# Kernel tuning notes

Hardware: AMD Instinct MI355X
Metric: run time of the kernel (lower is better)

## Reference

```python
import jax, jax.numpy as jnp
import numpy as np

CAP_FACTOR = 0.125  # capacity_factor from init_kwargs


def setup_inputs() -> dict:
    key = jax.random.key(0)
    k1, k2, k3, k4 = jax.random.split(key, 4)
    B, S, D, F = 4, 4096, 1024, 4096
    x = jax.random.normal(k1, (B, S, D), jnp.float32)
    w_router = jax.random.normal(k2, (D,), jnp.float32) * (D ** -0.5)
    W1 = jax.random.normal(k3, (D, F), jnp.float32) * (D ** -0.5)
    W2 = jax.random.normal(k4, (F, D), jnp.float32) * (F ** -0.5)
    return {"x": x, "w_router": w_router, "W1": W1, "W2": W2}


def reference(x, w_router, W1, W2):
    B, S, D = x.shape
    capacity = int(S * CAP_FACTOR)  # training-mode capacity (static)

    # router: Linear(dim,1,bias=False) + sigmoid -> [B, S]
    rw = jax.nn.sigmoid(jnp.einsum('bsd,d->bs', x, w_router))

    # topk over seq dim, then sort selected indices
    _, top_idx = jax.lax.top_k(rw, capacity)          # [B, cap]
    idx_sorted = jnp.sort(top_idx, axis=1)            # router_top_indices
    order = jnp.argsort(top_idx, axis=1)              # router_top_order (in [0, cap))

    # faithful to the original code: weights gathered from router_weights at
    # `order` positions (which index the first `capacity` sequence slots)
    w_top = jnp.take_along_axis(rw, order, axis=1)    # [B, cap]

    # gather selected tokens and run the submodule (gelu MLP)
    mod_x = jnp.take_along_axis(x, idx_sorted[:, :, None], axis=1)  # [B, cap, D]
    h = jax.nn.gelu(jnp.einsum('bcd,df->bcf', mod_x, W1))
    mod_out = jnp.einsum('bcf,fd->bcd', h, W2) * w_top[:, :, None]

    # scatter back to full sequence (indices are unique per batch)
    bidx = jnp.arange(B)[:, None]
    out = jnp.zeros_like(x).at[bidx, idx_sorted].set(mod_out)

    # BCE aux loss: targets are 1 at selected positions (log clamped at -100,
    # matching F.binary_cross_entropy)
    tgt = jnp.zeros_like(rw).at[bidx, idx_sorted].set(1.0)
    logw = jnp.maximum(jnp.log(rw), -100.0)
    log1mw = jnp.maximum(jnp.log1p(-rw), -100.0)
    mod_loss = -jnp.mean(tgt * logw + (1.0 - tgt) * log1mw)

    return out, mod_loss
```

## Files before the change

### kernel.cpp

```cpp
#include <hip/hip_runtime.h>
#include <stdint.h>

#define BB 4
#define SS 4096
#define DD 1024
#define FF 4096
#define CAP 512
#define MTOT (BB*CAP)
#define NOUT (BB*SS*DD)

typedef unsigned short ushort_t;
typedef float  float4v  __attribute__((ext_vector_type(4)));
typedef short  short8v  __attribute__((ext_vector_type(8)));
typedef unsigned short ushort4v __attribute__((ext_vector_type(4)));

#define OFF_RW   0u
#define OFF_IDX  (64u*1024u)
#define OFF_WTOP (72u*1024u)
#define OFF_LOSS (80u*1024u)
#define OFF_POS  (128u*1024u)
#define OFF_RANK (256u*1024u)
#define OFF_A    (1u<<20)
#define OFF_W1T  (5u<<20)
#define OFF_W2T  (13u<<20)
#define OFF_H    (21u<<20)
#define OFF_O    (37u<<20)

#define GLD16(gsrc, ldst) __builtin_amdgcn_global_load_lds( \
    (const __attribute__((address_space(1))) void*)(gsrc),  \
    (__attribute__((address_space(3))) void*)(ldst), 16, 0, 0)

__device__ inline ushort_t f2bf(float f) {
  uint32_t u = __builtin_bit_cast(uint32_t, f);
  u = u + 0x7fffu + ((u >> 16) & 1u);
  return (ushort_t)(u >> 16);
}
__device__ inline float bf2f(ushort_t h) {
  uint32_t u = (uint32_t)h << 16;
  return __builtin_bit_cast(float, u);
}

__global__ void router_kernel(const float* __restrict__ x, const float* __restrict__ w,
                              float* __restrict__ rw) {
  int wave = threadIdx.x >> 6;
  int lane = threadIdx.x & 63;
  int row  = blockIdx.x * 4 + wave;
  const float4* xr = (const float4*)(x + (size_t)row * DD);
  const float4* wr = (const float4*)w;
  float s = 0.f;
#pragma unroll
  for (int i = 0; i < 4; i++) {
    float4 a = xr[lane + i * 64];
    float4 b = wr[lane + i * 64];
    s += a.x * b.x + a.y * b.y + a.z * b.z + a.w * b.w;
  }
#pragma unroll
  for (int off = 32; off > 0; off >>= 1) s += __shfl_xor(s, off, 64);
  if (lane == 0) rw[row] = 1.f / (1.f + expf(-s));
}

__global__ __launch_bounds__(256) void rank_kernel(const float* __restrict__ rw,
                                                   int* __restrict__ rank) {
  __shared__ float v[SS];
  const int b = blockIdx.y;
  const float* rwg = rw + (size_t)b * SS;
  for (int m = threadIdx.x; m < SS / 4; m += 256)
    ((float4*)v)[m] = ((const float4*)rwg)[m];
  __syncthreads();
  const int e = blockIdx.x * 64 + (threadIdx.x >> 2);
  const int part = threadIdx.x & 3;
  const float vi = v[e];
  const int j0 = part * (SS / 4);
  int cnt = 0;
#pragma unroll 4
  for (int j4 = 0; j4 < SS / 16; ++j4) {
    float4 w = ((const float4*)(v + j0))[j4];
    int j = j0 + j4 * 4;
    cnt += (w.x > vi || (w.x == vi && (j + 0) < e));
    cnt += (w.y > vi || (w.y == vi && (j + 1) < e));
    cnt += (w.z > vi || (w.z == vi && (j + 2) < e));
    cnt += (w.w > vi || (w.w == vi && (j + 3) < e));
  }
  cnt += __shfl_xor(cnt, 1, 64);
  cnt += __shfl_xor(cnt, 2, 64);
  if (part == 0) rank[(size_t)b * SS + e] = cnt;
}

__global__ __launch_bounds__(1024) void finalize_kernel(const float* __restrict__ rw,
                                                        const int* __restrict__ rank,
                                                        int* __restrict__ idxs,
                                                        float* __restrict__ wtop,
                                                        int* __restrict__ posmap,
                                                        float* __restrict__ lossP) {
  __shared__ int   wsumI[16];
  __shared__ float wsumF[16];
  const int b = blockIdx.x, tid = threadIdx.x;
  const int lane = tid & 63, wv = tid >> 6;
  const float* rwg = rw + (size_t)b * SS;
  const int*   rkg = rank + (size_t)b * SS;
  const int m0 = tid * 4;
  int rk[4]; float rv[4];
  int cnt = 0;
#pragma unroll
  for (int u = 0; u < 4; u++) {
    rk[u] = rkg[m0 + u]; rv[u] = rwg[m0 + u];
    cnt += (rk[u] < CAP);
  }
  int val = cnt;
#pragma unroll
  for (int off = 1; off < 64; off <<= 1) {
    int n = __shfl_up(val, off, 64);
    if (lane >= off) val += n;
  }
  if (lane == 63) wsumI[wv] = val;
  __syncthreads();
  int wbase = 0;
  for (int w = 0; w < wv; ++w) wbase += wsumI[w];
  int excl = wbase + val - cnt;
#pragma unroll
  for (int u = 0; u < 4; u++) {
    int m = m0 + u;
    if (rk[u] < CAP) {
      int pos = excl++;
      idxs[b * CAP + pos] = m;
      wtop[b * CAP + pos] = rwg[rk[u]];
      posmap[(size_t)b * SS + m] = b * CAP + pos;
    } else {
      posmap[(size_t)b * SS + m] = -1;
    }
  }
  float ls = 0.f;
#pragma unroll
  for (int u = 0; u < 4; u++) {
    float term = (rk[u] < CAP) ? logf(rv[u]) : log1pf(-rv[u]);
    ls += fmaxf(term, -100.f);
  }
#pragma unroll
  for (int off = 32; off > 0; off >>= 1) ls += __shfl_xor(ls, off, 64);
  if (lane == 0) wsumF[wv] = ls;
  __syncthreads();
  if (tid == 0) {
    float t = 0.f;
    for (int i = 0; i < 16; i++) t += wsumF[i];
    lossP[b] = t;
  }
}

__global__ __launch_bounds__(256) void prep_kernel(const float* __restrict__ W1,
                                                   ushort_t* __restrict__ W1T,
                                                   const float* __restrict__ W2,
                                                   ushort_t* __restrict__ W2T,
                                                   const float* __restrict__ x,
                                                   const int* __restrict__ idxs,
                                                   ushort_t* __restrict__ A) {
  int id = blockIdx.x;
  const int tid = threadIdx.x;
  if (id < 8192) {
    __shared__ float t[32][33];
    const float* in; ushort_t* out; int R, C, bx, by;
    if (id < (FF / 32) * (DD / 32)) {
      in = W1; out = W1T; R = DD; C = FF;
      bx = id % (FF / 32); by = id / (FF / 32);
    } else {
      id -= (FF / 32) * (DD / 32);
      in = W2; out = W2T; R = FF; C = DD;
      bx = id % (DD / 32); by = id / (DD / 32);
    }
    const int c0 = bx * 32, r0 = by * 32;
    const int tx = tid & 7;
    const int ty = tid >> 3;
    const float4 vv = *(const float4*)&in[(size_t)(r0 + ty) * C + c0 + tx * 4];
    t[ty][tx * 4 + 0] = vv.x; t[ty][tx * 4 + 1] = vv.y;
    t[ty][tx * 4 + 2] = vv.z; t[ty][tx * 4 + 3] = vv.w;
    __syncthreads();
    ushort4v o;
    o[0] = f2bf(t[tx * 4 + 0][ty]); o[1] = f2bf(t[tx * 4 + 1][ty]);
    o[2] = f2bf(t[tx * 4 + 2][ty]); o[3] = f2bf(t[tx * 4 + 3][ty]);
    *(ushort4v*)&out[(size_t)(c0 + ty) * R + r0 + tx * 4] = o;
  } else {
    int row = id - 8192;
    int b = row >> 9;
    int seq = idxs[row];
    const float4* src = (const float4*)(x + ((size_t)(b * SS + seq)) * DD);
    float4 a = src[tid];
    ushort4v o;
    o[0] = f2bf(a.x); o[1] = f2bf(a.y); o[2] = f2bf(a.z); o[3] = f2bf(a.w);
    *(ushort4v*)(A + (size_t)row * DD + tid * 4) = o;
  }
}

__global__ void scatter_kernel(const ushort_t* __restrict__ O, const int* __restrict__ posmap,
                               const float* __restrict__ wtop, const float* __restrict__ lossP,
                               float* __restrict__ out) {
  int r = blockIdx.x;
  int p = posmap[r];
  float4 v = {0.f, 0.f, 0.f, 0.f};
  if (p >= 0) {
    float wt = wtop[p];
    const size_t stride = (size_t)MTOT * DD;
    const size_t off = (size_t)p * DD + threadIdx.x * 4;
    ushort4v h0 = *(const ushort4v*)(O + off);
    ushort4v h1 = *(const ushort4v*)(O + stride + off);
    ushort4v h2 = *(const ushort4v*)(O + 2 * stride + off);
    ushort4v h3 = *(const ushort4v*)(O + 3 * stride + off);
    v.x = ((bf2f(h0[0]) + bf2f(h1[0])) + (bf2f(h2[0]) + bf2f(h3[0]))) * wt;
    v.y = ((bf2f(h0[1]) + bf2f(h1[1])) + (bf2f(h2[1]) + bf2f(h3[1]))) * wt;
    v.z = ((bf2f(h0[2]) + bf2f(h1[2])) + (bf2f(h2[2]) + bf2f(h3[2]))) * wt;
    v.w = ((bf2f(h0[3]) + bf2f(h1[3])) + (bf2f(h2[3]) + bf2f(h3[3]))) * wt;
  }
  ((float4*)(out + (size_t)r * DD))[threadIdx.x] = v;
  if (r == 0 && threadIdx.x == 0)
    out[NOUT] = -(lossP[0] + lossP[1] + lossP[2] + lossP[3]) / (float)(BB * SS);
}

template <int MODE>
__global__ __launch_bounds__(256) void gemm_oc(const ushort_t* __restrict__ Ag,
                                               const ushort_t* __restrict__ Bg, int Kstride,
                                               ushort_t* __restrict__ Hout,
                                               ushort_t* __restrict__ Oacc) {
  __shared__ ushort_t lA[2][64 * 64];
  __shared__ ushort_t lB[2][64 * 64];
  const int tid = threadIdx.x;
  const int lane = tid & 63, wv = tid >> 6;
  const int wr = wv >> 1, wc = wv & 1;

  const int gx = gridDim.x, gy = gridDim.y;
  const int id = blockIdx.x + gx * (blockIdx.y + gy * blockIdx.z);
  const int xcd = id & 7, q = id >> 3;

  int bm0, bn0, bz, kbeg;
  if (MODE == 0) {
    const int mx = (xcd & 1) * 16 + (q & 15);
    const int nx = (xcd >> 1) * 16 + (q >> 4);
    bm0 = mx * 64; bn0 = nx * 64; bz = 0; kbeg = 0;
  } else {
    bz = xcd >> 1;
    const int by = (xcd & 1) * 16 + (q & 15);
    const int bx = q >> 4;
    bm0 = by * 64; bn0 = bx * 64; kbeg = bz * (Kstride >> 2);
  }
  const int kchunk = (MODE == 0) ? Kstride : (Kstride >> 2);
  const int nkt = kchunk / 128;

  const int srow = lane >> 3;
  const int gslot = (lane & 7) ^ srow;

  float4v acc[2][2];
#pragma unroll
  for (int i = 0; i < 2; i++)
#pragma unroll
    for (int j = 0; j < 2; j++) acc[i][j] = (float4v){0.f, 0.f, 0.f, 0.f};

  for (int t = 0; t < nkt; ++t) {
    const int k0 = kbeg + t * 128;
    __syncthreads();
#pragma unroll
    for (int p = 0; p < 2; p++) {
#pragma unroll
      for (int i = 0; i < 2; i++) {
        const int row = i * 32 + wv * 8 + srow;
        const int chunkbase = i * 256 + wv * 64;
        GLD16(Ag + (size_t)(bm0 + row) * Kstride + k0 + p * 64 + gslot * 8, &lA[p][chunkbase * 8]);
        GLD16(Bg + (size_t)(bn0 + row) * Kstride + k0 + p * 64 + gslot * 8, &lB[p][chunkbase * 8]);
      }
    }
    __syncthreads();
#pragma unroll
    for (int kk = 0; kk < 4; kk++) {
      const int pl = kk >> 1;
      const int s = (lane >> 4) + (kk & 1) * 4;
      short8v af[2], bfr[2];
#pragma unroll
      for (int mi = 0; mi < 2; mi++) {
        const int rr = wr * 32 + mi * 16 + (lane & 15);
        af[mi] = *(const short8v*)&lA[pl][rr * 64 + (s ^ (rr & 7)) * 8];
      }
#pragma unroll
      for (int nj = 0; nj < 2; nj++) {
        const int rr = wc * 32 + nj * 16 + (lane & 15);
        bfr[nj] = *(const short8v*)&lB[pl][rr * 64 + (s ^ (rr & 7)) * 8];
      }
#pragma unroll
      for (int mi = 0; mi < 2; mi++)
#pragma unroll
        for (int nj = 0; nj < 2; nj++)
          acc[mi][nj] = __builtin_amdgcn_mfma_f32_16x16x32_bf16(af[mi], bfr[nj], acc[mi][nj], 0, 0, 0);
    }
  }

  if (MODE == 0) {
#pragma unroll
    for (int mi = 0; mi < 2; mi++) {
      int r0 = bm0 + wr * 32 + mi * 16 + ((lane >> 4) << 2);
#pragma unroll
      for (int nj = 0; nj < 2; nj++) {
        int cc = bn0 + wc * 32 + nj * 16 + (lane & 15);
#pragma unroll
        for (int r = 0; r < 4; r++) {
          float xv = acc[mi][nj][r];
          float u = 0.7978845608028654f * (xv + 0.044715f * xv * xv * xv);
          float g = xv / (1.f + __expf(-2.f * u));
          Hout[(size_t)(r0 + r) * FF + cc] = f2bf(g);
        }
      }
    }
  } else {
    ushort_t* Op = Oacc + (size_t)bz * MTOT * DD;
#pragma unroll
    for (int mi = 0; mi < 2; mi++) {
      int tr0 = bm0 + wr * 32 + mi * 16 + ((lane >> 4) << 2);
#pragma unroll
      for (int r = 0; r < 4; r++) {
        ushort_t* orow = Op + (size_t)(tr0 + r) * DD + bn0 + wc * 32 + (lane & 15);
#pragma unroll
        for (int nj = 0; nj < 2; nj++) orow[nj * 16] = f2bf(acc[mi][nj][r]);
      }
    }
  }
}

extern "C" void kernel_launch(void* const* d_in, const int* in_sizes, int n_in,
                              void* d_out, int out_size, void* d_ws, size_t ws_size,
                              hipStream_t stream) {
  (void)in_sizes; (void)n_in; (void)out_size; (void)ws_size;
  const float* x  = (const float*)d_in[0];
  const float* wrt = (const float*)d_in[1];
  const float* W1 = (const float*)d_in[2];
  const float* W2 = (const float*)d_in[3];
  float* out = (float*)d_out;
  char* ws = (char*)d_ws;
  float*    rw   = (float*)(ws + OFF_RW);
  int*      idxs = (int*)(ws + OFF_IDX);
  float*    wtop = (float*)(ws + OFF_WTOP);
  float*    lossP= (float*)(ws + OFF_LOSS);
  int*      posm = (int*)(ws + OFF_POS);
  int*      rnk  = (int*)(ws + OFF_RANK);
  ushort_t* A    = (ushort_t*)(ws + OFF_A);
  ushort_t* W1T  = (ushort_t*)(ws + OFF_W1T);
  ushort_t* W2T  = (ushort_t*)(ws + OFF_W2T);
  ushort_t* H    = (ushort_t*)(ws + OFF_H);
  ushort_t* O    = (ushort_t*)(ws + OFF_O);

  router_kernel<<<dim3(BB * SS / 4), dim3(256), 0, stream>>>(x, wrt, rw);
  rank_kernel<<<dim3(SS / 64, BB), dim3(256), 0, stream>>>(rw, rnk);
  finalize_kernel<<<dim3(BB), dim3(1024), 0, stream>>>(rw, rnk, idxs, wtop, posm, lossP);
  prep_kernel<<<dim3(8192 + MTOT), dim3(256), 0, stream>>>(W1, W1T, W2, W2T, x, idxs, A);
  gemm_oc<0><<<dim3(FF / 64, MTOT / 64, 1), dim3(256), 0, stream>>>(A, W1T, DD, H, nullptr);
  gemm_oc<1><<<dim3(DD / 64, MTOT / 64, 4), dim3(256), 0, stream>>>(H, W2T, FF, nullptr, O);
  scatter_kernel<<<dim3(BB * SS), dim3(256), 0, stream>>>(O, posm, wtop, lossP, out);
}
```

Before: 125.9 us.

## Double-buffer GEMM LDS tiles to overlap global loads with MFMA

The GEMM main loop now uses the two LDS buffers as a ping-pong pair of 64-wide K tiles instead of loading one 128-wide tile into both and then computing. The next tile is prefetched via direct global-to-LDS loads while MFMAs consume the current one, with one waitcnt plus barrier per iteration. This aims to hide global load latency behind compute. The cost is twice as many loop iterations and barriers per K range. Inline s_barrier without a compiler-level fence could risk LDS read/write ordering.

```diff
diff --git a/kernel.cpp b/kernel.cpp
--- a/kernel.cpp
+++ b/kernel.cpp
@@ -240,7 +240,7 @@
     bm0 = by * 64; bn0 = bx * 64; kbeg = bz * (Kstride >> 2);
   }
   const int kchunk = (MODE == 0) ? Kstride : (Kstride >> 2);
-  const int nkt = kchunk / 128;
+  const int nkt = kchunk / 64;
 
   const int srow = lane >> 3;
   const int gslot = (lane & 7) ^ srow;
@@ -251,34 +251,37 @@
 #pragma unroll
     for (int j = 0; j < 2; j++) acc[i][j] = (float4v){0.f, 0.f, 0.f, 0.f};
 
+#define STAGE(buf, k0)                                                              \
+  {                                                                                 \
+    _Pragma("unroll")                                                               \
+    for (int i = 0; i < 2; i++) {                                                   \
+      const int row = i * 32 + wv * 8 + srow;                                       \
+      const int chunkbase = i * 256 + wv * 64;                                      \
+      GLD16(Ag + (size_t)(bm0 + row) * Kstride + (k0) + gslot * 8, &lA[buf][chunkbase * 8]); \
+      GLD16(Bg + (size_t)(bn0 + row) * Kstride + (k0) + gslot * 8, &lB[buf][chunkbase * 8]); \
+    }                                                                               \
+  }
+
+  STAGE(0, kbeg);
+  asm volatile("s_waitcnt vmcnt(0)" ::: "memory");
+  asm volatile("s_barrier" ::: "memory");
+
+  int cur = 0;
   for (int t = 0; t < nkt; ++t) {
-    const int k0 = kbeg + t * 128;
-    __syncthreads();
-#pragma unroll
-    for (int p = 0; p < 2; p++) {
-#pragma unroll
-      for (int i = 0; i < 2; i++) {
-        const int row = i * 32 + wv * 8 + srow;
-        const int chunkbase = i * 256 + wv * 64;
-        GLD16(Ag + (size_t)(bm0 + row) * Kstride + k0 + p * 64 + gslot * 8, &lA[p][chunkbase * 8]);
-        GLD16(Bg + (size_t)(bn0 + row) * Kstride + k0 + p * 64 + gslot * 8, &lB[p][chunkbase * 8]);
-      }
-    }
-    __syncthreads();
-#pragma unroll
-    for (int kk = 0; kk < 4; kk++) {
-      const int pl = kk >> 1;
-      const int s = (lane >> 4) + (kk & 1) * 4;
+    if (t + 1 < nkt) STAGE(cur ^ 1, kbeg + (t + 1) * 64);
+#pragma unroll
+    for (int kk = 0; kk < 2; kk++) {
+      const int s = (lane >> 4) + kk * 4;
       short8v af[2], bfr[2];
 #pragma unroll
       for (int mi = 0; mi < 2; mi++) {
         const int rr = wr * 32 + mi * 16 + (lane & 15);
-        af[mi] = *(const short8v*)&lA[pl][rr * 64 + (s ^ (rr & 7)) * 8];
+        af[mi] = *(const short8v*)&lA[cur][rr * 64 + (s ^ (rr & 7)) * 8];
       }
 #pragma unroll
       for (int nj = 0; nj < 2; nj++) {
         const int rr = wc * 32 + nj * 16 + (lane & 15);
-        bfr[nj] = *(const short8v*)&lB[pl][rr * 64 + (s ^ (rr & 7)) * 8];
+        bfr[nj] = *(const short8v*)&lB[cur][rr * 64 + (s ^ (rr & 7)) * 8];
       }
 #pragma unroll
       for (int mi = 0; mi < 2; mi++)
@@ -286,7 +289,13 @@
         for (int nj = 0; nj < 2; nj++)
           acc[mi][nj] = __builtin_amdgcn_mfma_f32_16x16x32_bf16(af[mi], bfr[nj], acc[mi][nj], 0, 0, 0);
     }
-  }
+    if (t + 1 < nkt) {
+      asm volatile("s_waitcnt vmcnt(0)" ::: "memory");
+      asm volatile("s_barrier" ::: "memory");
+    }
+    cur ^= 1;
+  }
+#undef STAGE
 
   if (MODE == 0) {
 #pragma unroll
```

New measurement: 127.0 us. About the same (+0.9%).
